# Kernel optimization log

Hardware: AMD Instinct MI355X
Metric: run time of the kernel (lower is better)

The kernel has to match this reference:

```python
import jax, jax.numpy as jnp
import numpy as np

N, IN_F, H, D = 3072, 512, 8, 64


def setup_inputs() -> dict:
    key = jax.random.key(0)
    k1, k2, k3, k4, k5 = jax.random.split(key, 5)
    x = jax.random.normal(k1, (N, IN_F), dtype=jnp.float32)
    adj = jax.random.randint(k2, (N, N), 0, 2, dtype=jnp.int32)
    # xavier-uniform-like scales
    s_W = (6.0 / (IN_F + H * D)) ** 0.5
    s_a = (6.0 / (H + D)) ** 0.5
    W = jax.random.uniform(k3, (H * D, IN_F), dtype=jnp.float32, minval=-s_W, maxval=s_W)
    a_src = jax.random.uniform(k4, (H, D), dtype=jnp.float32, minval=-s_a, maxval=s_a)
    a_dst = jax.random.uniform(k5, (H, D), dtype=jnp.float32, minval=-s_a, maxval=s_a)
    return {"x": x, "adj": adj, "W": W, "a_src": a_src, "a_dst": a_dst}


def reference(x, adj, W, a_src, a_dst):
    n = x.shape[0]
    Hh, d = a_src.shape
    h = (x @ W.T).reshape(n, Hh, d)                      # [n, H, d]
    e_src = jnp.einsum('nhd,hd->nh', h, a_src)           # [n, H]
    e_dst = jnp.einsum('nhd,hd->nh', h, a_dst)           # [n, H]
    e = e_src[:, None, :] + e_dst[None, :, :]            # [n, n, H], e[i,j]=src_i+dst_j
    e = jax.nn.leaky_relu(e, negative_slope=0.2)
    mask = (adj + jnp.eye(n, dtype=adj.dtype)) > 0       # [n, n]
    e = jnp.where(mask[:, :, None], e, -jnp.inf)
    alpha = jax.nn.softmax(e, axis=1)                    # softmax over j (neighbors)
    # out[i,h,d] = sum_j alpha[i,j,h] * h[j,h,d]  (dropout=0 / eval mode)
    out = jnp.einsum('ijh,jhd->ihd', alpha, h)
    return out.reshape(n, Hh * d)                        # concat=True
```

## Files before the change

### kernel.cpp

```cpp
#include <hip/hip_runtime.h>
#include <hip/hip_bf16.h>

typedef __bf16 bf16x8 __attribute__((ext_vector_type(8)));
typedef __bf16 bf16x4 __attribute__((ext_vector_type(4)));
typedef _Float16 half8 __attribute__((ext_vector_type(8)));
typedef _Float16 half4 __attribute__((ext_vector_type(4)));
typedef _Float16 half2v __attribute__((ext_vector_type(2)));
typedef float f32x4 __attribute__((ext_vector_type(4)));
typedef float f32x16 __attribute__((ext_vector_type(16)));

#define NROW 3072
#define NF 512
#define NH 8
#define ND 64

__device__ __forceinline__ unsigned gat_enc_key(float f) {
    unsigned u = __float_as_uint(f);
    return (f < 0.f) ? ~u : (u | 0x80000000u);
}
__device__ __forceinline__ float gat_dec_key(unsigned k) {
    unsigned u = (k & 0x80000000u) ? (k ^ 0x80000000u) : ~k;
    return __uint_as_float(u);
}

__global__ __launch_bounds__(256) void gat_prep(const float* __restrict__ x,
                                                const float* __restrict__ W,
                                                const int* __restrict__ adj,
                                                __bf16* __restrict__ xb,
                                                __bf16* __restrict__ Wb,
                                                unsigned long long* __restrict__ bits64,
                                                unsigned* __restrict__ maxkey) {
    if (blockIdx.x == 0 && threadIdx.x < NH) maxkey[threadIdx.x] = 0u;
    if (blockIdx.x < 1792) {
        int k = blockIdx.x * 256 + threadIdx.x;
        const float4* s; __bf16* d;
        if (k < 393216) { s = (const float4*)x; d = xb; }
        else { k -= 393216;  s = (const float4*)W; d = Wb; }
        float4 v = s[k];
        bf16x4 o = { (__bf16)v.x, (__bf16)v.y, (__bf16)v.z, (__bf16)v.w };
        *reinterpret_cast<bf16x4*>(d + k * 4) = o;
    } else {
        int i = blockIdx.x - 1792;
        int wave = threadIdx.x >> 6;
        int lane = threadIdx.x & 63;
        const int* row = adj + i * NROW;
#pragma unroll
        for (int it = 0; it < 12; ++it) {
            int base = wave * 768 + it * 64;
            int j = base + lane;
            bool pred = (row[j] > 0) || (j == i);
            unsigned long long bal = __ballot(pred);
            if (lane == 0) bits64[i * 48 + (base >> 6)] = bal;
        }
    }
}

__global__ __launch_bounds__(256) void gat_gemm(const __bf16* __restrict__ xb,
                                                const __bf16* __restrict__ Wb,
                                                _Float16* __restrict__ hT) {
    __shared__ _Float16 tile[4][16][17];
    int wave = threadIdx.x >> 6;
    int lane = threadIdx.x & 63;
    int t = blockIdx.x * 4 + wave;
    int i0 = (t >> 5) << 4;
    int o0 = (t & 31) << 4;
    int fr = lane & 15;
    int quad = lane >> 4;

    const bf16x8* xa = reinterpret_cast<const bf16x8*>(xb + (i0 + fr) * NF + quad * 8);
    const bf16x8* wp = reinterpret_cast<const bf16x8*>(Wb + (o0 + fr) * NF + quad * 8);

    f32x4 acc = {0.f, 0.f, 0.f, 0.f};
#pragma unroll
    for (int k = 0; k < 16; ++k) {
        bf16x8 a = xa[k * 4];
        bf16x8 b = wp[k * 4];
        acc = __builtin_amdgcn_mfma_f32_16x16x32_bf16(a, b, acc, 0, 0, 0);
    }
#pragma unroll
    for (int r = 0; r < 4; ++r)
        tile[wave][quad * 4 + r][fr] = (_Float16)acc[r];
    __syncthreads();
    int orow = lane >> 2;
    int li = (lane & 3) * 4;
    half4 o4 = { tile[wave][li][orow], tile[wave][li + 1][orow],
                 tile[wave][li + 2][orow], tile[wave][li + 3][orow] };
    *reinterpret_cast<half4*>(hT + (o0 + orow) * NROW + i0 + li) = o4;
}

__global__ __launch_bounds__(256) void gat_edges(const _Float16* __restrict__ hT,
                                                 const float* __restrict__ a_src,
                                                 const float* __restrict__ a_dst,
                                                 float* __restrict__ e_srcT,
                                                 float* __restrict__ e_dstT,
                                                 unsigned* __restrict__ maxkey) {
    int hh = blockIdx.y;
    int i = blockIdx.x * 256 + threadIdx.x;
    float ps = 0.f, pd = 0.f;
#pragma unroll
    for (int d = 0; d < ND; ++d) {
        float hv = (float)hT[(hh * ND + d) * NROW + i];
        ps += hv * a_src[hh * ND + d];
        pd += hv * a_dst[hh * ND + d];
    }
    e_srcT[hh * NROW + i] = ps;
    e_dstT[hh * NROW + i] = pd;
    float mx = pd;
#pragma unroll
    for (int off = 1; off < 64; off <<= 1) mx = fmaxf(mx, __shfl_xor(mx, off, 64));
    if ((threadIdx.x & 63) == 0) atomicMax(&maxkey[hh], gat_enc_key(mx));
}

__global__ __launch_bounds__(256) void gat_attn(const unsigned* __restrict__ bits,
                                                const float* __restrict__ e_srcT,
                                                const float* __restrict__ e_dstT,
                                                const unsigned* __restrict__ maxkey,
                                                const _Float16* __restrict__ hT,
                                                _Float16* __restrict__ num,
                                                float* __restrict__ den) {
    constexpr int JCHUNK = NROW / 4;
    constexpr int NC = JCHUNK / 64;
    __shared__ unsigned lds_P[JCHUNK / 2];
    __shared__ unsigned lds_Q[JCHUNK / 2];
    __shared__ __align__(16) _Float16 hbuf[2][4096];
    int b = blockIdx.x;
    int head = b & 7;
    int jc = (b >> 3) & 3;
    int i0 = ((b >> 3) >> 2) * 128;
    int jbase = jc * JCHUNK;
    int tid = threadIdx.x;
    int wave = tid >> 6;
    int lane = tid & 63;
    int half = lane >> 5;
    int l31 = lane & 31;

    float Mg = gat_dec_key(maxkey[head]);
    for (int p = tid; p < JCHUNK / 2; p += 256) {
        float t0 = e_dstT[head * NROW + jbase + 2 * p] - Mg;
        float t1 = e_dstT[head * NROW + jbase + 2 * p + 1] - Mg;
        half2v P = { (_Float16)__expf(t0), (_Float16)__expf(t1) };
        half2v Q = { (_Float16)__expf(0.2f * t0), (_Float16)__expf(0.2f * t1) };
        lds_P[p] = __builtin_bit_cast(unsigned, P);
        lds_Q[p] = __builtin_bit_cast(unsigned, Q);
    }

    int irow = i0 + wave * 32 + l31;
    float u = e_srcT[head * NROW + irow] + Mg;
    float Af = (u > 0.f) ? 1.f : __expf(0.8f * u);
    float Cf = (u > 0.f) ? __expf(-0.8f * u) : 1.f;
    _Float16 Ah = (_Float16)Af, Ch = (_Float16)Cf;
    half2v A2 = { Ah, Ah };
    half2v C2 = { Ch, Ch };
    const half2v one2 = { (_Float16)1.f, (_Float16)1.f };
    const unsigned* brow = bits + irow * 96 + jc * (JCHUNK / 32);

    int s0 = tid, s1 = tid + 256;
    const _Float16* gp0 = hT + (head * ND + ((s0 >> 6) & 1) * 32 + (s0 & 31)) * NROW
                             + jbase + (s0 >> 7) * 16 + ((s0 >> 5) & 1) * 8;
    const _Float16* gp1 = hT + (head * ND + ((s1 >> 6) & 1) * 32 + (s1 & 31)) * NROW
                             + jbase + (s1 >> 7) * 16 + ((s1 >> 5) & 1) * 8;
    *reinterpret_cast<half8*>(&hbuf[0][tid * 8])         = *reinterpret_cast<const half8*>(gp0);
    *reinterpret_cast<half8*>(&hbuf[0][(tid + 256) * 8]) = *reinterpret_cast<const half8*>(gp1);
    __syncthreads();

    f32x16 acc0 = {};
    f32x16 acc1 = {};
    float lsum = 0.f;
    uint2 wm = *reinterpret_cast<const uint2*>(brow);

    for (int k = 0; k < NC; ++k) {
        half8 st0, st1;
        uint2 wmn = wm;
        bool more = (k + 1 < NC);
        if (more) {
            st0 = *reinterpret_cast<const half8*>(gp0 + (k + 1) * 64);
            st1 = *reinterpret_cast<const half8*>(gp1 + (k + 1) * 64);
            wmn = *reinterpret_cast<const uint2*>(brow + (k + 1) * 2);
        }
        const _Float16* hb = &hbuf[k & 1][0];
#pragma unroll
        for (int js = 0; js < 4; ++js) {
            unsigned word = (js < 2) ? wm.x : wm.y;
            unsigned w8 = (word >> ((js & 1) * 16 + half * 8)) & 0xffu;
            uint4 Pv = *reinterpret_cast<const uint4*>(&lds_P[k * 32 + js * 8 + half * 4]);
            uint4 Qv = *reinterpret_cast<const uint4*>(&lds_Q[k * 32 + js * 8 + half * 4]);
            unsigned pr[4] = { Pv.x, Pv.y, Pv.z, Pv.w };
            unsigned qr[4] = { Qv.x, Qv.y, Qv.z, Qv.w };
            unsigned am[4];
#pragma unroll
            for (int t = 0; t < 4; ++t) {
                half2v pp = __builtin_bit_cast(half2v, pr[t]) * A2;
                half2v qq = __builtin_bit_cast(half2v, qr[t]) * C2;
                half2v mx = __builtin_elementwise_max(pp, qq);
                int b0 = ((int)(w8 << (31 - 2 * t))) >> 31;
                int b1 = ((int)(w8 << (30 - 2 * t))) >> 31;
                unsigned mk = ((unsigned)b0 & 0xFFFFu) | ((unsigned)b1 & 0xFFFF0000u);
                unsigned mr = __builtin_bit_cast(unsigned, mx) & mk;
                am[t] = mr;
                lsum = __builtin_amdgcn_fdot2(__builtin_bit_cast(half2v, mr), one2,
                                              lsum, false);
            }
            uint4 m4 = { am[0], am[1], am[2], am[3] };
            half8 af = __builtin_bit_cast(half8, m4);
            half8 v0 = *reinterpret_cast<const half8*>(hb + (js * 128 + lane) * 8);
            half8 v1 = *reinterpret_cast<const half8*>(hb + (js * 128 + 64 + lane) * 8);
            acc0 = __builtin_amdgcn_mfma_f32_32x32x16_f16(af, v0, acc0, 0, 0, 0);
            acc1 = __builtin_amdgcn_mfma_f32_32x32x16_f16(af, v1, acc1, 0, 0, 0);
        }
        if (more) {
            *reinterpret_cast<half8*>(&hbuf[(k + 1) & 1][tid * 8])         = st0;
            *reinterpret_cast<half8*>(&hbuf[(k + 1) & 1][(tid + 256) * 8]) = st1;
        }
        wm = wmn;
        __syncthreads();
    }

    lsum += __shfl_xor(lsum, 32, 64);
    if (half == 0)
        den[(jc * NROW + irow) * NH + head] = lsum;

#pragma unroll
    for (int reg = 0; reg < 16; ++reg) {
        int rowl = (reg & 3) + 8 * (reg >> 2) + 4 * half;
        long ob = (long)(jc * NROW + i0 + wave * 32 + rowl) * NF + head * ND + l31;
        num[ob]      = (_Float16)acc0[reg];
        num[ob + 32] = (_Float16)acc1[reg];
    }
}

__global__ __launch_bounds__(256) void gat_final(const _Float16* __restrict__ num,
                                                 const float* __restrict__ den,
                                                 float* __restrict__ out) {
    int idx = (blockIdx.x * 256 + threadIdx.x) * 8;
    int i = idx >> 9;
    int c = idx & 511;
    int head = c >> 6;
    half8 n0 = *reinterpret_cast<const half8*>(num + (long)i * NF + c);
    half8 n1 = *reinterpret_cast<const half8*>(num + (long)(NROW + i) * NF + c);
    half8 n2 = *reinterpret_cast<const half8*>(num + (long)(2 * NROW + i) * NF + c);
    half8 n3 = *reinterpret_cast<const half8*>(num + (long)(3 * NROW + i) * NF + c);
    float ds = den[i * NH + head] + den[(NROW + i) * NH + head]
             + den[(2 * NROW + i) * NH + head] + den[(3 * NROW + i) * NH + head];
    float inv = 1.0f / fmaxf(ds, 1e-30f);
    float r0 = ((float)n0[0] + (float)n1[0] + (float)n2[0] + (float)n3[0]) * inv;
    float r1 = ((float)n0[1] + (float)n1[1] + (float)n2[1] + (float)n3[1]) * inv;
    float r2 = ((float)n0[2] + (float)n1[2] + (float)n2[2] + (float)n3[2]) * inv;
    float r3 = ((float)n0[3] + (float)n1[3] + (float)n2[3] + (float)n3[3]) * inv;
    float r4 = ((float)n0[4] + (float)n1[4] + (float)n2[4] + (float)n3[4]) * inv;
    float r5 = ((float)n0[5] + (float)n1[5] + (float)n2[5] + (float)n3[5]) * inv;
    float r6 = ((float)n0[6] + (float)n1[6] + (float)n2[6] + (float)n3[6]) * inv;
    float r7 = ((float)n0[7] + (float)n1[7] + (float)n2[7] + (float)n3[7]) * inv;
    float4 o0 = { r0, r1, r2, r3 };
    float4 o1 = { r4, r5, r6, r7 };
    *reinterpret_cast<float4*>(out + idx)     = o0;
    *reinterpret_cast<float4*>(out + idx + 4) = o1;
}

extern "C" void kernel_launch(void* const* d_in, const int* in_sizes, int n_in,
                              void* d_out, int out_size, void* d_ws, size_t ws_size,
                              hipStream_t stream) {
    const float* x_raw  = (const float*)d_in[0];
    const int*   adj    = (const int*)d_in[1];
    const float* W_raw  = (const float*)d_in[2];
    const float* as_raw = (const float*)d_in[3];
    const float* ad_raw = (const float*)d_in[4];
    float* out = (float*)d_out;

    char* ws = (char*)d_ws;
    _Float16* hT     = (_Float16*)(ws);
    float*    e_srcT = (float*)(ws + 3145728);
    float*    e_dstT = (float*)(ws + 3244032);
    unsigned* maxkey = (unsigned*)(ws + 3342336);
    unsigned* bits   = (unsigned*)(ws + 3342400);
    __bf16*   xb     = (__bf16*)(ws + 4522048);
    __bf16*   Wb     = (__bf16*)(ws + 7667776);
    _Float16* num    = (_Float16*)(ws + 8192064);
    float*    den    = (float*)(ws + 20774976);

    gat_prep<<<4864, 256, 0, stream>>>(x_raw, W_raw, adj, xb, Wb,
                                       (unsigned long long*)bits, maxkey);
    gat_gemm<<<1536, 256, 0, stream>>>(xb, Wb, hT);
    gat_edges<<<dim3(12, 8), 256, 0, stream>>>(hT, as_raw, ad_raw, e_srcT, e_dstT, maxkey);
    gat_attn<<<24 * 4 * 8, 256, 0, stream>>>(bits, e_srcT, e_dstT, maxkey, hT, num, den);
    gat_final<<<NROW * NF / 2048, 256, 0, stream>>>(num, den, out);
}
```

Baseline: 147.9 us.

## Tile GEMM through LDS, fuse adjacency bitpacking into it, compute denominators via MFMA

Replaces the per-wave 16x16 GEMM, which reloads its operands straight from global memory, with a 64x64 block-tiled GEMM. It stages swizzled, double-buffered tiles in shared memory and uses 32x32x16 bf16 MFMA. The adjacency bit-packing moves from the prep kernel into extra blocks of the GEMM launch, so the bandwidth-bound bitpacking overlaps with the compute-bound GEMM. In the attention kernel, the softmax denominator is now accumulated by a third MFMA against a ones vector instead of per-lane fdot2 plus a shuffle. This frees VALU work at the cost of extra MFMA issue and accumulator registers.

After: 140.7 us. 1.05x faster.

```diff
diff --git a/kernel.cpp b/kernel.cpp
--- a/kernel.cpp
+++ b/kernel.cpp
@@ -13,6 +13,7 @@
 #define NF 512
 #define NH 8
 #define ND 64
+#define GEMM_BLOCKS 384
 
 __device__ __forceinline__ unsigned gat_enc_key(float f) {
     unsigned u = __float_as_uint(f);
@@ -25,22 +26,29 @@
 
 __global__ __launch_bounds__(256) void gat_prep(const float* __restrict__ x,
                                                 const float* __restrict__ W,
-                                                const int* __restrict__ adj,
                                                 __bf16* __restrict__ xb,
                                                 __bf16* __restrict__ Wb,
-                                                unsigned long long* __restrict__ bits64,
                                                 unsigned* __restrict__ maxkey) {
     if (blockIdx.x == 0 && threadIdx.x < NH) maxkey[threadIdx.x] = 0u;
-    if (blockIdx.x < 1792) {
-        int k = blockIdx.x * 256 + threadIdx.x;
-        const float4* s; __bf16* d;
-        if (k < 393216) { s = (const float4*)x; d = xb; }
-        else { k -= 393216;  s = (const float4*)W; d = Wb; }
-        float4 v = s[k];
-        bf16x4 o = { (__bf16)v.x, (__bf16)v.y, (__bf16)v.z, (__bf16)v.w };
-        *reinterpret_cast<bf16x4*>(d + k * 4) = o;
-    } else {
-        int i = blockIdx.x - 1792;
+    int k = blockIdx.x * 256 + threadIdx.x;
+    const float4* s; __bf16* d;
+    if (k < 393216) { s = (const float4*)x; d = xb; }
+    else { k -= 393216;  s = (const float4*)W; d = Wb; }
+    float4 v = s[k];
+    bf16x4 o = { (__bf16)v.x, (__bf16)v.y, (__bf16)v.z, (__bf16)v.w };
+    *reinterpret_cast<bf16x4*>(d + k * 4) = o;
+}
+
+__global__ __launch_bounds__(256) void gat_gemm_bp(const __bf16* __restrict__ xb,
+                                                   const __bf16* __restrict__ Wb,
+                                                   _Float16* __restrict__ hT,
+                                                   const int* __restrict__ adj,
+                                                   unsigned long long* __restrict__ bits64) {
+    __shared__ __align__(16) __bf16 sA[2][4096];
+    __shared__ __align__(16) __bf16 sB[2][4096];
+
+    if (blockIdx.x >= GEMM_BLOCKS) {
+        int i = blockIdx.x - GEMM_BLOCKS;
         int wave = threadIdx.x >> 6;
         int lane = threadIdx.x & 63;
         const int* row = adj + i * NROW;
@@ -52,40 +60,90 @@
             unsigned long long bal = __ballot(pred);
             if (lane == 0) bits64[i * 48 + (base >> 6)] = bal;
         }
-    }
-}
-
-__global__ __launch_bounds__(256) void gat_gemm(const __bf16* __restrict__ xb,
-                                                const __bf16* __restrict__ Wb,
-                                                _Float16* __restrict__ hT) {
-    __shared__ _Float16 tile[4][16][17];
-    int wave = threadIdx.x >> 6;
-    int lane = threadIdx.x & 63;
-    int t = blockIdx.x * 4 + wave;
-    int i0 = (t >> 5) << 4;
-    int o0 = (t & 31) << 4;
-    int fr = lane & 15;
-    int quad = lane >> 4;
-
-    const bf16x8* xa = reinterpret_cast<const bf16x8*>(xb + (i0 + fr) * NF + quad * 8);
-    const bf16x8* wp = reinterpret_cast<const bf16x8*>(Wb + (o0 + fr) * NF + quad * 8);
-
-    f32x4 acc = {0.f, 0.f, 0.f, 0.f};
-#pragma unroll
-    for (int k = 0; k < 16; ++k) {
-        bf16x8 a = xa[k * 4];
-        bf16x8 b = wp[k * 4];
-        acc = __builtin_amdgcn_mfma_f32_16x16x32_bf16(a, b, acc, 0, 0, 0);
-    }
-#pragma unroll
-    for (int r = 0; r < 4; ++r)
-        tile[wave][quad * 4 + r][fr] = (_Float16)acc[r];
+        return;
+    }
+
+    int b = blockIdx.x;
+    int i0 = (b >> 3) * 64;
+    int o0 = (b & 7) * 64;
+    int tid = threadIdx.x;
+    int wave = tid >> 6;
+    int lane = tid & 63;
+    int half = lane >> 5;
+    int l31 = lane & 31;
+    int wr = wave >> 1;
+    int wc = wave & 1;
+
+    int v0 = tid, v1 = tid + 256;
+    int r0 = v0 >> 3, r1 = v1 >> 3;
+    int cc0 = ((v0 & 7) ^ (r0 & 7)) << 3;
+    int cc1 = ((v1 & 7) ^ (r1 & 7)) << 3;
+    const __bf16* gA0 = xb + (i0 + r0) * NF + cc0;
+    const __bf16* gA1 = xb + (i0 + r1) * NF + cc1;
+    const __bf16* gB0 = Wb + (o0 + r0) * NF + cc0;
+    const __bf16* gB1 = Wb + (o0 + r1) * NF + cc1;
+
+    {
+        bf16x8 a0 = *reinterpret_cast<const bf16x8*>(gA0);
+        bf16x8 a1 = *reinterpret_cast<const bf16x8*>(gA1);
+        bf16x8 b0 = *reinterpret_cast<const bf16x8*>(gB0);
+        bf16x8 b1 = *reinterpret_cast<const bf16x8*>(gB1);
+        *reinterpret_cast<bf16x8*>(&sA[0][v0 * 8]) = a0;
+        *reinterpret_cast<bf16x8*>(&sA[0][v1 * 8]) = a1;
+        *reinterpret_cast<bf16x8*>(&sB[0][v0 * 8]) = b0;
+        *reinterpret_cast<bf16x8*>(&sB[0][v1 * 8]) = b1;
+    }
     __syncthreads();
-    int orow = lane >> 2;
-    int li = (lane & 3) * 4;
-    half4 o4 = { tile[wave][li][orow], tile[wave][li + 1][orow],
-                 tile[wave][li + 2][orow], tile[wave][li + 3][orow] };
-    *reinterpret_cast<half4*>(hT + (o0 + orow) * NROW + i0 + li) = o4;
+
+    f32x16 acc = {};
+    int arow = (wr * 32 + l31) * 64;
+    int brow = (wc * 32 + l31) * 64;
+    int sw7 = l31 & 7;
+
+    for (int c = 0; c < 8; ++c) {
+        bf16x8 na0, na1, nb0, nb1;
+        bool more = (c < 7);
+        if (more) {
+            na0 = *reinterpret_cast<const bf16x8*>(gA0 + (c + 1) * 64);
+            na1 = *reinterpret_cast<const bf16x8*>(gA1 + (c + 1) * 64);
+            nb0 = *reinterpret_cast<const bf16x8*>(gB0 + (c + 1) * 64);
+            nb1 = *reinterpret_cast<const bf16x8*>(gB1 + (c + 1) * 64);
+        }
+        const __bf16* pa = &sA[c & 1][0];
+        const __bf16* pb = &sB[c & 1][0];
+#pragma unroll
+        for (int ks = 0; ks < 4; ++ks) {
+            int q = (((ks << 1) | half) ^ sw7) << 3;
+            bf16x8 a = *reinterpret_cast<const bf16x8*>(pa + arow + q);
+            bf16x8 bb = *reinterpret_cast<const bf16x8*>(pb + brow + q);
+            acc = __builtin_amdgcn_mfma_f32_32x32x16_bf16(a, bb, acc, 0, 0, 0);
+        }
+        if (more) {
+            *reinterpret_cast<bf16x8*>(&sA[(c + 1) & 1][v0 * 8]) = na0;
+            *reinterpret_cast<bf16x8*>(&sA[(c + 1) & 1][v1 * 8]) = na1;
+            *reinterpret_cast<bf16x8*>(&sB[(c + 1) & 1][v0 * 8]) = nb0;
+            *reinterpret_cast<bf16x8*>(&sB[(c + 1) & 1][v1 * 8]) = nb1;
+        }
+        __syncthreads();
+    }
+
+    _Float16* tt = reinterpret_cast<_Float16*>(&sA[0][0]) + wave * 1056;
+#pragma unroll
+    for (int reg = 0; reg < 16; ++reg) {
+        int rowl = (reg & 3) + 8 * (reg >> 2) + 4 * half;
+        tt[rowl * 33 + l31] = (_Float16)acc[reg];
+    }
+    __syncthreads();
+    int orow = lane >> 1;
+    int li = (lane & 1) * 16;
+    half8 h0, h1;
+#pragma unroll
+    for (int t = 0; t < 8; ++t) h0[t] = tt[(li + t) * 33 + orow];
+#pragma unroll
+    for (int t = 0; t < 8; ++t) h1[t] = tt[(li + 8 + t) * 33 + orow];
+    _Float16* op = hT + (long)(o0 + wc * 32 + orow) * NROW + i0 + wr * 32 + li;
+    *reinterpret_cast<half8*>(op) = h0;
+    *reinterpret_cast<half8*>(op + 8) = h1;
 }
 
 __global__ __launch_bounds__(256) void gat_edges(const _Float16* __restrict__ hT,
@@ -151,7 +209,8 @@
     _Float16 Ah = (_Float16)Af, Ch = (_Float16)Cf;
     half2v A2 = { Ah, Ah };
     half2v C2 = { Ch, Ch };
-    const half2v one2 = { (_Float16)1.f, (_Float16)1.f };
+    const half8 ones8 = { (_Float16)1.f, (_Float16)1.f, (_Float16)1.f, (_Float16)1.f,
+                          (_Float16)1.f, (_Float16)1.f, (_Float16)1.f, (_Float16)1.f };
     const unsigned* brow = bits + irow * 96 + jc * (JCHUNK / 32);
 
     int s0 = tid, s1 = tid + 256;
@@ -165,7 +224,7 @@
 
     f32x16 acc0 = {};
     f32x16 acc1 = {};
-    float lsum = 0.f;
+    f32x16 acc2 = {};
     uint2 wm = *reinterpret_cast<const uint2*>(brow);
 
     for (int k = 0; k < NC; ++k) {
@@ -195,10 +254,7 @@
                 int b0 = ((int)(w8 << (31 - 2 * t))) >> 31;
                 int b1 = ((int)(w8 << (30 - 2 * t))) >> 31;
                 unsigned mk = ((unsigned)b0 & 0xFFFFu) | ((unsigned)b1 & 0xFFFF0000u);
-                unsigned mr = __builtin_bit_cast(unsigned, mx) & mk;
-                am[t] = mr;
-                lsum = __builtin_amdgcn_fdot2(__builtin_bit_cast(half2v, mr), one2,
-                                              lsum, false);
+                am[t] = __builtin_bit_cast(unsigned, mx) & mk;
             }
             uint4 m4 = { am[0], am[1], am[2], am[3] };
             half8 af = __builtin_bit_cast(half8, m4);
@@ -206,6 +262,7 @@
             half8 v1 = *reinterpret_cast<const half8*>(hb + (js * 128 + 64 + lane) * 8);
             acc0 = __builtin_amdgcn_mfma_f32_32x32x16_f16(af, v0, acc0, 0, 0, 0);
             acc1 = __builtin_amdgcn_mfma_f32_32x32x16_f16(af, v1, acc1, 0, 0, 0);
+            acc2 = __builtin_amdgcn_mfma_f32_32x32x16_f16(af, ones8, acc2, 0, 0, 0);
         }
         if (more) {
             *reinterpret_cast<half8*>(&hbuf[(k + 1) & 1][tid * 8])         = st0;
@@ -215,9 +272,13 @@
         __syncthreads();
     }
 
-    lsum += __shfl_xor(lsum, 32, 64);
-    if (half == 0)
-        den[(jc * NROW + irow) * NH + head] = lsum;
+    if (l31 == 0) {
+#pragma unroll
+        for (int reg = 0; reg < 16; ++reg) {
+            int rowl = (reg & 3) + 8 * (reg >> 2) + 4 * half;
+            den[(long)(jc * NROW + i0 + wave * 32 + rowl) * NH + head] = acc2[reg];
+        }
+    }
 
 #pragma unroll
     for (int reg = 0; reg < 16; ++reg) {
@@ -277,9 +338,9 @@
     _Float16* num    = (_Float16*)(ws + 8192064);
     float*    den    = (float*)(ws + 20774976);
 
-    gat_prep<<<4864, 256, 0, stream>>>(x_raw, W_raw, adj, xb, Wb,
-                                       (unsigned long long*)bits, maxkey);
-    gat_gemm<<<1536, 256, 0, stream>>>(xb, Wb, hT);
+    gat_prep<<<1792, 256, 0, stream>>>(x_raw, W_raw, xb, Wb, maxkey);
+    gat_gemm_bp<<<GEMM_BLOCKS + NROW, 256, 0, stream>>>(xb, Wb, hT, adj,
+                                                        (unsigned long long*)bits);
     gat_edges<<<dim3(12, 8), 256, 0, stream>>>(hT, as_raw, ad_raw, e_srcT, e_dstT, maxkey);
     gat_attn<<<24 * 4 * 8, 256, 0, stream>>>(bits, e_srcT, e_dstT, maxkey, hT, num, den);
     gat_final<<<NROW * NF / 2048, 256, 0, stream>>>(num, den, out);
```
